# Kernel tuning notes

Measured on AMD Instinct MI355X. Metric: run time of the kernel, lower is better.

Reference implementation:

```python
import jax, jax.numpy as jnp
import numpy as np

B = 524288  # number of mel frames
MEL = 128   # mel bins (hard-coded in module)
D = 64      # code dim
K = 128     # codebook size


def setup_inputs() -> dict:
    key = jax.random.key(0)
    ks = jax.random.split(key, 7)
    return {
        "mel_frame": jax.random.normal(ks[0], (B, MEL), dtype=jnp.float32),
        "W_in": jax.random.normal(ks[1], (D, MEL), dtype=jnp.float32) * 0.05,
        "b_in": jax.random.normal(ks[2], (D,), dtype=jnp.float32) * 0.05,
        "cb0": jax.random.normal(ks[3], (K, D), dtype=jnp.float32),
        "cb1": jax.random.normal(ks[4], (K, D), dtype=jnp.float32),
        "W_out": jax.random.normal(ks[5], (MEL, D), dtype=jnp.float32) * 0.05,
        "b_out": jax.random.normal(ks[6], (MEL,), dtype=jnp.float32) * 0.05,
    }


def reference(mel_frame, W_in, b_in, cb0, cb1, W_out, b_out):
    # encode: project mel -> d, then greedy residual VQ over 2 codebooks
    z = mel_frame @ W_in.T + b_in                      # (B, D)
    residual = z
    z_q = jnp.zeros_like(z)
    idxs = []
    for cb in (cb0, cb1):
        # squared L2 distance without materializing (B, K, D):
        # ||r - c||^2 = ||r||^2 - 2 r.c + ||c||^2  -> (B, K)
        dist = (
            jnp.sum(residual * residual, axis=-1, keepdims=True)
            - 2.0 * (residual @ cb.T)
            + jnp.sum(cb * cb, axis=-1)
        )
        ind = jnp.argmin(dist, axis=-1)                # (B,)
        code = cb[ind]                                 # gather chosen codes (B, D)
        residual = residual - code
        z_q = z_q + code
        idxs.append(ind)
    # decode: sum of selected codes -> project back to mel
    mel = z_q @ W_out.T + b_out                        # (B, MEL)
    return mel, jnp.stack(idxs, axis=-1)
```

## Files before the change

### kernel.cpp

```cpp
#include <hip/hip_runtime.h>
#include <hip/hip_bf16.h>

#define B_ROWS   524288
#define MEL_BINS 128
#define DIM      64
#define KCODES   128

#define WS_WT 0
#define WS_N0 (WS_WT + MEL_BINS*DIM)
#define WS_N1 (WS_N0 + KCODES)
#define WS_T0 (WS_N1 + KCODES)
#define WS_T1 (WS_T0 + KCODES*MEL_BINS)
#define WS_TOT (WS_T1 + KCODES*MEL_BINS)

__device__ __forceinline__ float np_pairwise64_sq(const float* v) {
#pragma clang fp contract(off)
    float r0 = v[0]*v[0], r1 = v[1]*v[1], r2 = v[2]*v[2], r3 = v[3]*v[3];
    float r4 = v[4]*v[4], r5 = v[5]*v[5], r6 = v[6]*v[6], r7 = v[7]*v[7];
#pragma unroll
    for (int i = 8; i < 64; i += 8) {
        r0 += v[i+0]*v[i+0]; r1 += v[i+1]*v[i+1];
        r2 += v[i+2]*v[i+2]; r3 += v[i+3]*v[i+3];
        r4 += v[i+4]*v[i+4]; r5 += v[i+5]*v[i+5];
        r6 += v[i+6]*v[i+6]; r7 += v[i+7]*v[i+7];
    }
    return ((r0 + r1) + (r2 + r3)) + ((r4 + r5) + (r6 + r7));
}

__global__ __launch_bounds__(256) void rvq_precomp(
    const float* __restrict__ W_in, const float* __restrict__ cb0,
    const float* __restrict__ cb1, const float* __restrict__ W_out,
    float* __restrict__ ws)
{
#pragma clang fp contract(off)
    float* WT = ws + WS_WT;
    float* n0 = ws + WS_N0;
    float* n1 = ws + WS_N1;
    float* T0 = ws + WS_T0;
    float* T1 = ws + WS_T1;

    int tid = blockIdx.x * 256 + threadIdx.x;
    if (tid < 16384) {
        int i = tid >> 7, m = tid & 127;
        double a = 0.0;
        for (int d = 0; d < DIM; ++d)
            a = fma((double)cb0[i*DIM + d], (double)W_out[m*DIM + d], a);
        T0[tid] = (float)a;
    } else if (tid < 32768) {
        int t = tid - 16384;
        int i = t >> 7, m = t & 127;
        double a = 0.0;
        for (int d = 0; d < DIM; ++d)
            a = fma((double)cb1[i*DIM + d], (double)W_out[m*DIM + d], a);
        T1[t] = (float)a;
    } else if (tid < 40960) {
        int t = tid - 32768;
        int j = t >> 6, d = t & 63;
        WT[t] = W_in[d*MEL_BINS + j];
    } else if (tid < 41216) {
        int t = tid - 40960;
        const float* cb = (t & 128) ? cb1 : cb0;
        float*       nn = (t & 128) ? n1  : n0;
        int k = t & 127;
        nn[k] = np_pairwise64_sq(cb + k*DIM);
    }
}

__global__ __launch_bounds__(256) void rvq_main(
    const float* __restrict__ mel,
    const float* __restrict__ b_in,
    const float* __restrict__ cb0,
    const float* __restrict__ cb1,
    const float* __restrict__ b_out,
    const float* __restrict__ ws,
    float* __restrict__ out_mel,
    float* __restrict__ out_idx)
{
#pragma clang fp contract(off)
    const float* __restrict__ WT = ws + WS_WT;
    const float* __restrict__ n0 = ws + WS_N0;
    const float* __restrict__ n1 = ws + WS_N1;
    const float* __restrict__ T0 = ws + WS_T0;
    const float* __restrict__ T1 = ws + WS_T1;

    const int b = blockIdx.x * 256 + threadIdx.x;

    float z[DIM];
#pragma unroll
    for (int d = 0; d < DIM; ++d) z[d] = 0.f;

    const float4* melr = reinterpret_cast<const float4*>(mel + (size_t)b * MEL_BINS);
    for (int jc = 0; jc < MEL_BINS / 4; ++jc) {
        float4 m4 = melr[jc];
        const float* w = WT + jc * 4 * DIM;
#pragma unroll
        for (int d = 0; d < DIM; ++d) z[d] = fmaf(w[d],         m4.x, z[d]);
#pragma unroll
        for (int d = 0; d < DIM; ++d) z[d] = fmaf(w[DIM + d],   m4.y, z[d]);
#pragma unroll
        for (int d = 0; d < DIM; ++d) z[d] = fmaf(w[2*DIM + d], m4.z, z[d]);
#pragma unroll
        for (int d = 0; d < DIM; ++d) z[d] = fmaf(w[3*DIM + d], m4.w, z[d]);
    }
#pragma unroll
    for (int d = 0; d < DIM; ++d) z[d] = z[d] + b_in[d];

    float s0 = z[0]*z[0], s1 = z[1]*z[1], s2 = z[2]*z[2], s3 = z[3]*z[3];
    float s4 = z[4]*z[4], s5 = z[5]*z[5], s6 = z[6]*z[6], s7 = z[7]*z[7];
#pragma unroll
    for (int i = 8; i < 64; i += 8) {
        s0 += z[i+0]*z[i+0]; s1 += z[i+1]*z[i+1];
        s2 += z[i+2]*z[i+2]; s3 += z[i+3]*z[i+3];
        s4 += z[i+4]*z[i+4]; s5 += z[i+5]*z[i+5];
        s6 += z[i+6]*z[i+6]; s7 += z[i+7]*z[i+7];
    }
    float sum_rr = ((s0 + s1) + (s2 + s3)) + ((s4 + s5) + (s6 + s7));

    float best0 = 3.4e38f; int i0 = 0;
#pragma unroll 2
    for (int k = 0; k < KCODES; ++k) {
        const float* c = cb0 + k * DIM;
        float acc = 0.f;
#pragma unroll
        for (int d = 0; d < DIM; ++d) acc = fmaf(c[d], z[d], acc);
        float dist = (sum_rr - 2.0f*acc) + n0[k];
        if (dist < best0) { best0 = dist; i0 = k; }
    }

    {
        const float* c = cb0 + (size_t)i0 * DIM;
#pragma unroll
        for (int d = 0; d < DIM; ++d) z[d] = z[d] - c[d];
    }

    s0 = z[0]*z[0]; s1 = z[1]*z[1]; s2 = z[2]*z[2]; s3 = z[3]*z[3];
    s4 = z[4]*z[4]; s5 = z[5]*z[5]; s6 = z[6]*z[6]; s7 = z[7]*z[7];
#pragma unroll
    for (int i = 8; i < 64; i += 8) {
        s0 += z[i+0]*z[i+0]; s1 += z[i+1]*z[i+1];
        s2 += z[i+2]*z[i+2]; s3 += z[i+3]*z[i+3];
        s4 += z[i+4]*z[i+4]; s5 += z[i+5]*z[i+5];
        s6 += z[i+6]*z[i+6]; s7 += z[i+7]*z[i+7];
    }
    sum_rr = ((s0 + s1) + (s2 + s3)) + ((s4 + s5) + (s6 + s7));

    float best1 = 3.4e38f; int i1 = 0;
#pragma unroll 2
    for (int k = 0; k < KCODES; ++k) {
        const float* c = cb1 + k * DIM;
        float acc = 0.f;
#pragma unroll
        for (int d = 0; d < DIM; ++d) acc = fmaf(c[d], z[d], acc);
        float dist = (sum_rr - 2.0f*acc) + n1[k];
        if (dist < best1) { best1 = dist; i1 = k; }
    }

    const float4* t0r = reinterpret_cast<const float4*>(T0 + (size_t)i0 * MEL_BINS);
    const float4* t1r = reinterpret_cast<const float4*>(T1 + (size_t)i1 * MEL_BINS);
    float4* outr = reinterpret_cast<float4*>(out_mel + (size_t)b * MEL_BINS);
#pragma unroll 4
    for (int q = 0; q < MEL_BINS / 4; ++q) {
        float4 a = t0r[q], c = t1r[q];
        float4 o;
        o.x = a.x + c.x + b_out[4*q + 0];
        o.y = a.y + c.y + b_out[4*q + 1];
        o.z = a.z + c.z + b_out[4*q + 2];
        o.w = a.w + c.w + b_out[4*q + 3];
        outr[q] = o;
    }

    out_idx[2*(size_t)b + 0] = (float)i0;
    out_idx[2*(size_t)b + 1] = (float)i1;
}

extern "C" void kernel_launch(void* const* d_in, const int* in_sizes, int n_in,
                              void* d_out, int out_size, void* d_ws, size_t ws_size,
                              hipStream_t stream)
{
    const float* mel   = (const float*)d_in[0];
    const float* W_in  = (const float*)d_in[1];
    const float* b_in  = (const float*)d_in[2];
    const float* cb0   = (const float*)d_in[3];
    const float* cb1   = (const float*)d_in[4];
    const float* W_out = (const float*)d_in[5];
    const float* b_out = (const float*)d_in[6];

    float* ws      = (float*)d_ws;
    float* out_mel = (float*)d_out;
    float* out_idx = (float*)d_out + (size_t)B_ROWS * MEL_BINS;

    rvq_precomp<<<(WS_TOT + 255) / 256, 256, 0, stream>>>(W_in, cb0, cb1, W_out, ws);
    rvq_main<<<B_ROWS / 256, 256, 0, stream>>>(mel, b_in, cb0, cb1, b_out, ws,
                                               out_mel, out_idx);
}
```

Baseline: 594.0 us.

## Stage projection weights and transposed codebooks in LDS for register-blocked distance scans

The input projection weights and both codebooks are now staged through shared memory in 16KB halves. Previously each thread read them from global or scalar memory per row. The codebooks are pre-transposed into 16-code panels in the precompute kernel, so each thread can compute 16 dot products at once with float4 LDS broadcast reads. This is meant to cut global/constant-cache traffic and raise ILP in the distance loops, at the cost of extra block barriers, 16KB of LDS per block, and more register pressure.

```diff
diff --git a/kernel.cpp b/kernel.cpp
--- a/kernel.cpp
+++ b/kernel.cpp
@@ -7,7 +7,9 @@
 #define KCODES   128
 
 #define WS_WT 0
-#define WS_N0 (WS_WT + MEL_BINS*DIM)
+#define WS_P0 (WS_WT + MEL_BINS*DIM)
+#define WS_P1 (WS_P0 + DIM*KCODES)
+#define WS_N0 (WS_P1 + DIM*KCODES)
 #define WS_N1 (WS_N0 + KCODES)
 #define WS_T0 (WS_N1 + KCODES)
 #define WS_T1 (WS_T0 + KCODES*MEL_BINS)
@@ -34,6 +36,8 @@
 {
 #pragma clang fp contract(off)
     float* WT = ws + WS_WT;
+    float* P0 = ws + WS_P0;
+    float* P1 = ws + WS_P1;
     float* n0 = ws + WS_N0;
     float* n1 = ws + WS_N1;
     float* T0 = ws + WS_T0;
@@ -63,6 +67,16 @@
         float*       nn = (t & 128) ? n1  : n0;
         int k = t & 127;
         nn[k] = np_pairwise64_sq(cb + k*DIM);
+    } else if (tid < 49408) {
+        int e = tid - 41216;
+        int c = e >> 10, rem = e & 1023;
+        int d = rem >> 4, t = rem & 15;
+        P0[e] = cb0[(c*16 + t)*DIM + d];
+    } else if (tid < 57600) {
+        int e = tid - 49408;
+        int c = e >> 10, rem = e & 1023;
+        int d = rem >> 4, t = rem & 15;
+        P1[e] = cb1[(c*16 + t)*DIM + d];
     }
 }
 
@@ -77,30 +91,46 @@
     float* __restrict__ out_idx)
 {
 #pragma clang fp contract(off)
-    const float* __restrict__ WT = ws + WS_WT;
-    const float* __restrict__ n0 = ws + WS_N0;
-    const float* __restrict__ n1 = ws + WS_N1;
-    const float* __restrict__ T0 = ws + WS_T0;
-    const float* __restrict__ T1 = ws + WS_T1;
-
-    const int b = blockIdx.x * 256 + threadIdx.x;
+    const float* __restrict__ n0g = ws + WS_N0;
+    const float* __restrict__ n1g = ws + WS_N1;
+    const float* __restrict__ T0  = ws + WS_T0;
+    const float* __restrict__ T1  = ws + WS_T1;
+
+    __shared__ float slds[4096];
+    float4* sw4 = reinterpret_cast<float4*>(slds);
+    const float4* sl4 = reinterpret_cast<const float4*>(slds);
+
+    const int tid = threadIdx.x;
+    const int b = blockIdx.x * 256 + tid;
+    const float4* melr = reinterpret_cast<const float4*>(mel + (size_t)b * MEL_BINS);
 
     float z[DIM];
 #pragma unroll
     for (int d = 0; d < DIM; ++d) z[d] = 0.f;
 
-    const float4* melr = reinterpret_cast<const float4*>(mel + (size_t)b * MEL_BINS);
-    for (int jc = 0; jc < MEL_BINS / 4; ++jc) {
-        float4 m4 = melr[jc];
-        const float* w = WT + jc * 4 * DIM;
-#pragma unroll
-        for (int d = 0; d < DIM; ++d) z[d] = fmaf(w[d],         m4.x, z[d]);
-#pragma unroll
-        for (int d = 0; d < DIM; ++d) z[d] = fmaf(w[DIM + d],   m4.y, z[d]);
-#pragma unroll
-        for (int d = 0; d < DIM; ++d) z[d] = fmaf(w[2*DIM + d], m4.z, z[d]);
-#pragma unroll
-        for (int d = 0; d < DIM; ++d) z[d] = fmaf(w[3*DIM + d], m4.w, z[d]);
+    const float4* wt4 = reinterpret_cast<const float4*>(ws + WS_WT);
+    for (int h = 0; h < 2; ++h) {
+        __syncthreads();
+#pragma unroll
+        for (int i = 0; i < 4; ++i) sw4[i*256 + tid] = wt4[h*1024 + i*256 + tid];
+        __syncthreads();
+
+        for (int jc = 0; jc < 16; ++jc) {
+            float4 m4 = melr[h*16 + jc];
+#pragma unroll
+            for (int seg = 0; seg < 4; ++seg) {
+                float mj = (seg == 0) ? m4.x : (seg == 1) ? m4.y : (seg == 2) ? m4.z : m4.w;
+                const float4* w4 = sl4 + (jc*4 + seg)*16;
+#pragma unroll
+                for (int q = 0; q < 16; ++q) {
+                    float4 wv = w4[q];
+                    z[4*q + 0] = fmaf(wv.x, mj, z[4*q + 0]);
+                    z[4*q + 1] = fmaf(wv.y, mj, z[4*q + 1]);
+                    z[4*q + 2] = fmaf(wv.z, mj, z[4*q + 2]);
+                    z[4*q + 3] = fmaf(wv.w, mj, z[4*q + 3]);
+                }
+            }
+        }
     }
 #pragma unroll
     for (int d = 0; d < DIM; ++d) z[d] = z[d] + b_in[d];
@@ -116,21 +146,57 @@
     }
     float sum_rr = ((s0 + s1) + (s2 + s3)) + ((s4 + s5) + (s6 + s7));
 
+    const float4* p04 = reinterpret_cast<const float4*>(ws + WS_P0);
     float best0 = 3.4e38f; int i0 = 0;
-#pragma unroll 2
-    for (int k = 0; k < KCODES; ++k) {
-        const float* c = cb0 + k * DIM;
-        float acc = 0.f;
-#pragma unroll
-        for (int d = 0; d < DIM; ++d) acc = fmaf(c[d], z[d], acc);
-        float dist = (sum_rr - 2.0f*acc) + n0[k];
-        if (dist < best0) { best0 = dist; i0 = k; }
+    for (int h = 0; h < 2; ++h) {
+        __syncthreads();
+#pragma unroll
+        for (int i = 0; i < 4; ++i) sw4[i*256 + tid] = p04[h*1024 + i*256 + tid];
+        __syncthreads();
+
+        for (int q = 0; q < 4; ++q) {
+            const float4* pan = sl4 + q*256;
+            float acc[16];
+#pragma unroll
+            for (int t = 0; t < 16; ++t) acc[t] = 0.f;
+#pragma unroll
+            for (int d = 0; d < DIM; ++d) {
+                float4 p0 = pan[d*4 + 0];
+                float4 p1 = pan[d*4 + 1];
+                float4 p2 = pan[d*4 + 2];
+                float4 p3 = pan[d*4 + 3];
+                float zd = z[d];
+                acc[ 0] = fmaf(p0.x, zd, acc[ 0]);
+                acc[ 1] = fmaf(p0.y, zd, acc[ 1]);
+                acc[ 2] = fmaf(p0.z, zd, acc[ 2]);
+                acc[ 3] = fmaf(p0.w, zd, acc[ 3]);
+                acc[ 4] = fmaf(p1.x, zd, acc[ 4]);
+                acc[ 5] = fmaf(p1.y, zd, acc[ 5]);
+                acc[ 6] = fmaf(p1.z, zd, acc[ 6]);
+                acc[ 7] = fmaf(p1.w, zd, acc[ 7]);
+                acc[ 8] = fmaf(p2.x, zd, acc[ 8]);
+                acc[ 9] = fmaf(p2.y, zd, acc[ 9]);
+                acc[10] = fmaf(p2.z, zd, acc[10]);
+                acc[11] = fmaf(p2.w, zd, acc[11]);
+                acc[12] = fmaf(p3.x, zd, acc[12]);
+                acc[13] = fmaf(p3.y, zd, acc[13]);
+                acc[14] = fmaf(p3.z, zd, acc[14]);
+                acc[15] = fmaf(p3.w, zd, acc[15]);
+            }
+            const int kb = h*64 + q*16;
+            const float* nk = n0g + kb;
+#pragma unroll
+            for (int t = 0; t < 16; ++t) {
+                float dist = (sum_rr - 2.0f*acc[t]) + nk[t];
+                if (dist < best0) { best0 = dist; i0 = kb + t; }
+            }
+        }
     }
 
     {
-        const float* c = cb0 + (size_t)i0 * DIM;
-#pragma unroll
-        for (int d = 0; d < DIM; ++d) z[d] = z[d] - c[d];
+        const float* cc = cb0 + (size_t)i0 * DIM;
+#pragma unroll
+        for (int d = 0; d < DIM; ++d) z[d] = z[d] - cc[d];
     }
 
     s0 = z[0]*z[0]; s1 = z[1]*z[1]; s2 = z[2]*z[2]; s3 = z[3]*z[3];
@@ -144,15 +210,51 @@
     }
     sum_rr = ((s0 + s1) + (s2 + s3)) + ((s4 + s5) + (s6 + s7));
 
+    const float4* p14 = reinterpret_cast<const float4*>(ws + WS_P1);
     float best1 = 3.4e38f; int i1 = 0;
-#pragma unroll 2
-    for (int k = 0; k < KCODES; ++k) {
-        const float* c = cb1 + k * DIM;
-        float acc = 0.f;
-#pragma unroll
-        for (int d = 0; d < DIM; ++d) acc = fmaf(c[d], z[d], acc);
-        float dist = (sum_rr - 2.0f*acc) + n1[k];
-        if (dist < best1) { best1 = dist; i1 = k; }
+    for (int h = 0; h < 2; ++h) {
+        __syncthreads();
+#pragma unroll
+        for (int i = 0; i < 4; ++i) sw4[i*256 + tid] = p14[h*1024 + i*256 + tid];
+        __syncthreads();
+
+        for (int q = 0; q < 4; ++q) {
+            const float4* pan = sl4 + q*256;
+            float acc[16];
+#pragma unroll
+            for (int t = 0; t < 16; ++t) acc[t] = 0.f;
+#pragma unroll
+            for (int d = 0; d < DIM; ++d) {
+                float4 p0 = pan[d*4 + 0];
+                float4 p1 = pan[d*4 + 1];
+                float4 p2 = pan[d*4 + 2];
+                float4 p3 = pan[d*4 + 3];
+                float zd = z[d];
+                acc[ 0] = fmaf(p0.x, zd, acc[ 0]);
+                acc[ 1] = fmaf(p0.y, zd, acc[ 1]);
+                acc[ 2] = fmaf(p0.z, zd, acc[ 2]);
+                acc[ 3] = fmaf(p0.w, zd, acc[ 3]);
+                acc[ 4] = fmaf(p1.x, zd, acc[ 4]);
+                acc[ 5] = fmaf(p1.y, zd, acc[ 5]);
+                acc[ 6] = fmaf(p1.z, zd, acc[ 6]);
+                acc[ 7] = fmaf(p1.w, zd, acc[ 7]);
+                acc[ 8] = fmaf(p2.x, zd, acc[ 8]);
+                acc[ 9] = fmaf(p2.y, zd, acc[ 9]);
+                acc[10] = fmaf(p2.z, zd, acc[10]);
+                acc[11] = fmaf(p2.w, zd, acc[11]);
+                acc[12] = fmaf(p3.x, zd, acc[12]);
+                acc[13] = fmaf(p3.y, zd, acc[13]);
+                acc[14] = fmaf(p3.z, zd, acc[14]);
+                acc[15] = fmaf(p3.w, zd, acc[15]);
+            }
+            const int kb = h*64 + q*16;
+            const float* nk = n1g + kb;
+#pragma unroll
+            for (int t = 0; t < 16; ++t) {
+                float dist = (sum_rr - 2.0f*acc[t]) + nk[t];
+                if (dist < best1) { best1 = dist; i1 = kb + t; }
+            }
+        }
     }
 
     const float4* t0r = reinterpret_cast<const float4*>(T0 + (size_t)i0 * MEL_BINS);
@@ -160,12 +262,12 @@
     float4* outr = reinterpret_cast<float4*>(out_mel + (size_t)b * MEL_BINS);
 #pragma unroll 4
     for (int q = 0; q < MEL_BINS / 4; ++q) {
-        float4 a = t0r[q], c = t1r[q];
+        float4 a = t0r[q], cc = t1r[q];
         float4 o;
-        o.x = a.x + c.x + b_out[4*q + 0];
-        o.y = a.y + c.y + b_out[4*q + 1];
-        o.z = a.z + c.z + b_out[4*q + 2];
-        o.w = a.w + c.w + b_out[4*q + 3];
+        o.x = a.x + cc.x + b_out[4*q + 0];
+        o.y = a.y + cc.y + b_out[4*q + 1];
+        o.z = a.z + cc.z + b_out[4*q + 2];
+        o.w = a.w + cc.w + b_out[4*q + 3];
         outr[q] = o;
     }
 
```

Result: faster. 516.5 us (-13.0%).
